# Optimization experiments

Measured on AMD Instinct MI355X. Metric: run time of the kernel, lower is better.

The kernel has to match this reference:

```python
import jax, jax.numpy as jnp
import numpy as np

B, Hh, Ww, C = 16, 56, 56, 256
NH, WS, SS = 8, 7, 3
HD = C // NH
N = WS * WS
SCALE = HD ** -0.5
EPS = 1e-5


def _rel_pos_index():
    coords = np.stack(np.meshgrid(np.arange(WS), np.arange(WS), indexing='ij'))  # (2, ws, ws)
    cf = coords.reshape(2, -1)
    rc = (cf[:, :, None] - cf[:, None, :]).transpose(1, 2, 0).astype(np.int64)  # (N, N, 2)
    rc[:, :, 0] += WS - 1
    rc[:, :, 1] += WS - 1
    rc[:, :, 0] *= 2 * WS - 1
    return jnp.asarray(rc.sum(-1))  # (N, N)

REL_IDX = _rel_pos_index()


def _shift_mask():
    # standard Swin SW-MSA mask for cyclic shift
    img = np.zeros((1, Hh, Ww, 1), dtype=np.float32)
    cnt = 0
    for hs in (slice(0, -WS), slice(-WS, -SS), slice(-SS, None)):
        for ws_ in (slice(0, -WS), slice(-WS, -SS), slice(-SS, None)):
            img[:, hs, ws_, :] = cnt
            cnt += 1
    mw = img.reshape(1, Hh // WS, WS, Ww // WS, WS, 1).transpose(0, 1, 3, 2, 4, 5).reshape(-1, N)
    am = mw[:, None, :] - mw[:, :, None]
    return jnp.asarray(np.where(am != 0, -100.0, 0.0).astype(np.float32))  # (nW, N, N)


def _ln(x, g, b):
    mu = x.mean(-1, keepdims=True)
    var = ((x - mu) ** 2).mean(-1, keepdims=True)
    return (x - mu) * jax.lax.rsqrt(var + EPS) * g + b


def setup_inputs() -> dict:
    key = jax.random.key(0)
    ks = jax.random.split(key, 8)
    return {
        'x': jax.random.normal(ks[0], (B, Hh * Ww, C), jnp.float32),
        'mask': _shift_mask(),
        'norm1_g': jnp.ones((C,), jnp.float32),
        'norm1_b': jnp.zeros((C,), jnp.float32),
        'qkv_w': jax.random.normal(ks[1], (3 * C, C), jnp.float32) * 0.02,
        'qkv_b': jnp.zeros((3 * C,), jnp.float32),
        'rel_bias': jax.random.normal(ks[2], ((2 * WS - 1) ** 2, NH), jnp.float32) * 0.02,
        'proj_w': jax.random.normal(ks[3], (C, C), jnp.float32) * 0.02,
        'proj_b': jnp.zeros((C,), jnp.float32),
        'norm2_g': jnp.ones((C,), jnp.float32),
        'norm2_b': jnp.zeros((C,), jnp.float32),
        'fc1_w': jax.random.normal(ks[4], (4 * C, C), jnp.float32) * 0.02,
        'fc1_b': jnp.zeros((4 * C,), jnp.float32),
        'fc2_w': jax.random.normal(ks[5], (C, 4 * C), jnp.float32) * 0.02,
        'fc2_b': jnp.zeros((C,), jnp.float32),
    }


def reference(x, mask, norm1_g, norm1_b, qkv_w, qkv_b, rel_bias, proj_w, proj_b,
              norm2_g, norm2_b, fc1_w, fc1_b, fc2_w, fc2_b):
    shortcut = x
    h = _ln(x, norm1_g, norm1_b).reshape(B, Hh, Ww, C)
    # cyclic shift
    h = jnp.roll(h, (-SS, -SS), axis=(1, 2))
    # window partition -> (B*nW, N, C)
    hw = h.reshape(B, Hh // WS, WS, Ww // WS, WS, C).transpose(0, 1, 3, 2, 4, 5).reshape(-1, N, C)
    # qkv projection
    qkv = (hw @ qkv_w.T + qkv_b).reshape(-1, N, 3, NH, HD).transpose(2, 0, 3, 1, 4)
    q, k, v = qkv[0] * SCALE, qkv[1], qkv[2]  # (Bw, NH, N, HD)
    attn = jnp.einsum('bhnd,bhmd->bhnm', q, k)  # (Bw, NH, N, N)
    rpb = rel_bias[REL_IDX.reshape(-1)].reshape(N, N, NH).transpose(2, 0, 1)
    attn = attn + rpb[None]
    nW = mask.shape[0]
    attn = attn.reshape(B, nW, NH, N, N) + mask[None, :, None]
    attn = jax.nn.softmax(attn.reshape(-1, NH, N, N), axis=-1)
    o = jnp.einsum('bhnm,bhmd->bhnd', attn, v).transpose(0, 2, 1, 3).reshape(-1, N, C)
    o = o @ proj_w.T + proj_b
    # window reverse
    o = o.reshape(B, Hh // WS, Ww // WS, WS, WS, C).transpose(0, 1, 3, 2, 4, 5).reshape(B, Hh, Ww, C)
    o = jnp.roll(o, (SS, SS), axis=(1, 2)).reshape(B, Hh * Ww, C)
    x = shortcut + o
    h2 = _ln(x, norm2_g, norm2_b)
    h2 = jax.nn.gelu(h2 @ fc1_w.T + fc1_b, approximate=False)
    return x + (h2 @ fc2_w.T + fc2_b)
```

## Files before the change

kernel.cpp:

```cpp
#include <hip/hip_runtime.h>
#include <cmath>

#define B_    16
#define HH    56
#define WWI   56
#define C_    256
#define NH_   8
#define WS_   7
#define SS_   3
#define HD_   32
#define NTOK  50176
#define NN    49
#define SCALE_ 0.17677669529663689f
#define EPS_  1e-5f

typedef __bf16  bf16x8  __attribute__((ext_vector_type(8)));
typedef float   f32x4   __attribute__((ext_vector_type(4)));
typedef unsigned short ushort8v __attribute__((ext_vector_type(8)));

__device__ __forceinline__ unsigned short f2bf(float f) {
    unsigned int u = __float_as_uint(f);
    unsigned int r = u + 0x7FFFu + ((u >> 16) & 1u);
    return (unsigned short)(r >> 16);
}
__device__ __forceinline__ float bf2f(unsigned short h) {
    return __uint_as_float(((unsigned int)h) << 16);
}
__device__ __forceinline__ float gelu_t(float x) {
    float t = 0.7978845608028654f * (x + 0.044715f * x * x * x);
    float e = __expf(2.0f * t);
    float th = 1.0f - 2.0f * __builtin_amdgcn_rcpf(e + 1.0f);
    return 0.5f * x * (1.0f + th);
}

__device__ __forceinline__ void gload_lds16(const unsigned short* g, unsigned short* l) {
    __builtin_amdgcn_global_load_lds(
        (const __attribute__((address_space(1))) unsigned int*)g,
        (__attribute__((address_space(3))) unsigned int*)l, 16, 0, 0);
}

__global__ __launch_bounds__(256) void prep_k(
    const float* __restrict__ qkvw, const float* __restrict__ projw,
    const float* __restrict__ fc1w, const float* __restrict__ fc2w,
    unsigned short* __restrict__ dst,
    const float* __restrict__ mask, const float* __restrict__ relb,
    unsigned short* __restrict__ cb)
{
    if (blockIdx.x < 3072) {
        int i = blockIdx.x * 256 + threadIdx.x;
        float v;
        if      (i < 196608) v = qkvw[i];
        else if (i < 262144) v = projw[i - 196608];
        else if (i < 524288) v = fc1w[i - 262144];
        else                 v = fc2w[i - 524288];
        dst[i] = f2bf(v);
    } else {
        int s = blockIdx.x - 3072;
        int wi = s >> 3, head = s & 7;
        for (int p = threadIdx.x; p < 2408; p += 256) {
            float v = 0.0f;
            if (p < 2401) {
                int i = p / NN, j = p - i * NN;
                int di = i / 7 - j / 7 + 6, dj = i % 7 - j % 7 + 6;
                v = relb[(di * 13 + dj) * NH_ + head] + mask[(size_t)wi * 2401 + p];
            }
            cb[(size_t)s * 2408 + p] = f2bf(v);
        }
    }
}

__global__ __launch_bounds__(256) void ln_k(
    const float* __restrict__ x, const float* __restrict__ g,
    const float* __restrict__ bta, unsigned short* __restrict__ dst, int shifted)
{
    int wave = threadIdx.x >> 6, lane = threadIdx.x & 63;
    int tok = blockIdx.x * 4 + wave;
    const float4 v = *(const float4*)(x + (size_t)tok * C_ + lane * 4);
    float s = v.x + v.y + v.z + v.w;
    float q = v.x*v.x + v.y*v.y + v.z*v.z + v.w*v.w;
    for (int o = 32; o > 0; o >>= 1) { s += __shfl_xor(s, o, 64); q += __shfl_xor(q, o, 64); }
    float mu  = s * (1.0f / C_);
    float var = q * (1.0f / C_) - mu * mu;
    float rs  = rsqrtf(var + EPS_);
    float4 gg = *(const float4*)(g   + lane * 4);
    float4 bb = *(const float4*)(bta + lane * 4);
    float y0 = (v.x - mu) * rs * gg.x + bb.x;
    float y1 = (v.y - mu) * rs * gg.y + bb.y;
    float y2 = (v.z - mu) * rs * gg.z + bb.z;
    float y3 = (v.w - mu) * rs * gg.w + bb.w;
    size_t di;
    if (shifted) {
        int b = tok / 3136, p = tok % 3136;
        int ph = p / 56, pw = p % 56;
        int sh = ph - SS_; if (sh < 0) sh += HH;
        int sw = pw - SS_; if (sw < 0) sw += WWI;
        int bw = b * 64 + (sh / WS_) * 8 + (sw / WS_);
        int n  = (sh % WS_) * WS_ + (sw % WS_);
        di = ((size_t)bw * NN + n) * C_ + lane * 4;
    } else {
        di = (size_t)tok * C_ + lane * 4;
    }
    unsigned int lo = (unsigned int)f2bf(y0) | ((unsigned int)f2bf(y1) << 16);
    unsigned int hi = (unsigned int)f2bf(y2) | ((unsigned int)f2bf(y3) << 16);
    uint2 u; u.x = lo; u.y = hi;
    *(uint2*)(dst + di) = u;
}

template<int EPI, int NT>
__global__ __launch_bounds__(256, 4) void gemm_k(
    const unsigned short* __restrict__ A, const unsigned short* __restrict__ Bt,
    int K, const float* __restrict__ bias,
    const float* __restrict__ resid, float* __restrict__ outF,
    unsigned short* __restrict__ outQ, unsigned short* __restrict__ outK,
    unsigned short* __restrict__ outV)
{
    __shared__ __align__(16) unsigned char smem[32768];
    const int tid = threadIdx.x;
    const int lin = blockIdx.x;
    const int xcd = lin & 7, t = lin >> 3;
    const int m0 = (xcd * 49 + t / NT) * 128;
    const int n0 = (t % NT) * 128;
    const int wave = tid >> 6, lane = tid & 63, quad = lane >> 4, l16 = lane & 15;
    const int wm = wave >> 1, wn = wave & 1;
    const int r0 = tid >> 2;
    const int c0 = (((tid & 3) ^ ((tid >> 3) & 3)) * 8);

    const size_t gA0 = (size_t)(m0 + r0) * K + c0;
    const size_t gA1 = (size_t)(m0 + r0 + 64) * K + c0;
    const size_t gB0 = (size_t)(n0 + r0) * K + c0;
    const size_t gB1 = (size_t)(n0 + r0 + 64) * K + c0;
    const int woff = wave * 512;
    const int sw8 = (quad ^ ((l16 >> 1) & 3)) * 8;

    f32x4 acc[4][4] = {};
    const int nk = K >> 5;

    #define STAGE(kt_, p_) { \
        unsigned short* sA_ = (unsigned short*)(smem + (p_) * 16384); \
        unsigned short* sB_ = sA_ + 4096; \
        const int kp_ = (kt_) << 5; \
        gload_lds16(A + gA0 + kp_, sA_ + woff); \
        gload_lds16(A + gA1 + kp_, sA_ + woff + 2048); \
        gload_lds16(Bt + gB0 + kp_, sB_ + woff); \
        gload_lds16(Bt + gB1 + kp_, sB_ + woff + 2048); }

    STAGE(0, 0);
    for (int kk = 0; kk < nk; ++kk) {
        const int p = kk & 1;
        if (kk + 1 < nk) {
            STAGE(kk + 1, p ^ 1);
            __asm volatile("s_waitcnt vmcnt(4)\n\ts_barrier" ::: "memory");
        } else {
            __asm volatile("s_waitcnt vmcnt(0)\n\ts_barrier" ::: "memory");
        }
        const unsigned short* sA = (const unsigned short*)(smem + p * 16384);
        const unsigned short* sB = sA + 4096;
        bf16x8 af[4], bfr[4];
        #pragma unroll
        for (int tt = 0; tt < 4; ++tt) {
            af[tt]  = __builtin_bit_cast(bf16x8, *(const ushort8v*)(sA + (wm * 64 + tt * 16 + l16) * 32 + sw8));
            bfr[tt] = __builtin_bit_cast(bf16x8, *(const ushort8v*)(sB + (wn * 64 + tt * 16 + l16) * 32 + sw8));
        }
        #pragma unroll
        for (int mt = 0; mt < 4; ++mt)
            #pragma unroll
            for (int nt = 0; nt < 4; ++nt)
                acc[mt][nt] = __builtin_amdgcn_mfma_f32_16x16x32_bf16(af[mt], bfr[nt], acc[mt][nt], 0, 0, 0);
        __asm volatile("s_barrier" ::: "memory");
    }
    #undef STAGE

    float b4[4];
    #pragma unroll
    for (int nt = 0; nt < 4; ++nt) b4[nt] = bias[n0 + wn * 64 + nt * 16 + l16];

    if (EPI == 0 || EPI == 2) {
        unsigned short (*swB)[136] = (unsigned short (*)[136])smem;
        const int seg = n0 >> 8;
        const float qs = (EPI == 0 && seg == 0) ? SCALE_ : 1.0f;
        #pragma unroll
        for (int p = 0; p < 2; ++p) {
            __syncthreads();
            if (wm == p) {
                #pragma unroll
                for (int mt = 0; mt < 4; ++mt)
                    #pragma unroll
                    for (int nt = 0; nt < 4; ++nt)
                        #pragma unroll
                        for (int r = 0; r < 4; ++r) {
                            float v = acc[mt][nt][r] + b4[nt];
                            if (EPI == 0) v *= qs; else v = gelu_t(v);
                            swB[mt * 16 + quad * 4 + r][wn * 64 + nt * 16 + l16] = f2bf(v);
                        }
            }
            __syncthreads();
            if (EPI == 0) {
                unsigned short* dstp = seg == 0 ? outQ : (seg == 1 ? outK : outV);
                const int nbase = n0 & 255;
                for (int tt = tid; tt < 1024; tt += 256) {
                    int row = tt >> 4, c8 = (tt & 15) * 8;
                    int m = m0 + p * 64 + row, bw = m / NN, nw = m - bw * NN;
                    int cc = nbase + c8;
                    uint4 u = *(uint4*)&swB[row][c8];
                    *(uint4*)&dstp[(((size_t)bw * NH_ + (cc >> 5)) * NN + nw) * HD_ + (cc & 31)] = u;
                }
            } else {
                for (int tt = tid; tt < 1024; tt += 256) {
                    int row = tt >> 4, c8 = (tt & 15) * 8;
                    uint4 u = *(uint4*)&swB[row][c8];
                    *(uint4*)&outQ[(size_t)(m0 + p * 64 + row) * 1024 + n0 + c8] = u;
                }
            }
        }
    } else {
        float (*swF)[132] = (float (*)[132])smem;
        #pragma unroll
        for (int p = 0; p < 4; ++p) {
            __syncthreads();
            if (wm == (p >> 1)) {
                const int mtb = (p & 1) * 2;
                #pragma unroll
                for (int mt = 0; mt < 2; ++mt)
                    #pragma unroll
                    for (int nt = 0; nt < 4; ++nt)
                        #pragma unroll
                        for (int r = 0; r < 4; ++r)
                            swF[mt * 16 + quad * 4 + r][wn * 64 + nt * 16 + l16] =
                                acc[mtb + mt][nt][r] + b4[nt];
            }
            __syncthreads();
            for (int tt = tid; tt < 1024; tt += 256) {
                int rl = tt >> 5, c4 = (tt & 31) * 4;
                size_t adr;
                if (EPI == 1) {
                    int m = m0 + p * 32 + rl, bw = m / NN, nw = m - bw * NN;
                    int b = bw >> 6, wi = bw & 63;
                    int sh = (wi >> 3) * WS_ + nw / WS_;
                    int sw = (wi & 7) * WS_ + nw % WS_;
                    int ph = sh + SS_; if (ph >= HH)  ph -= HH;
                    int pw = sw + SS_; if (pw >= WWI) pw -= WWI;
                    adr = ((size_t)b * 3136 + ph * 56 + pw) * C_ + n0 + c4;
                } else {
                    adr = (size_t)(m0 + p * 32 + rl) * C_ + n0 + c4;
                }
                float4 u = *(float4*)&swF[rl][c4];
                const float4 rr = (EPI == 1) ? *(const float4*)&resid[adr]
                                             : *(const float4*)&outF[adr];
                u.x += rr.x; u.y += rr.y; u.z += rr.z; u.w += rr.w;
                *(float4*)&outF[adr] = u;
            }
        }
    }
}

__global__ __launch_bounds__(256) void attn_k(
    const unsigned short* __restrict__ qb, const unsigned short* __restrict__ kb,
    const unsigned short* __restrict__ vb, const unsigned short* __restrict__ cb,
    unsigned short* __restrict__ ob)
{
    __shared__ unsigned short qs[64][40];
    __shared__ unsigned short ks[64][40];
    __shared__ unsigned short vt[32][72];
    __shared__ unsigned short sp[64][72];
    __shared__ unsigned short cbs[2408];
    const int tid = threadIdx.x;
    const int bw = blockIdx.x >> 3, head = blockIdx.x & 7;
    const size_t base = (size_t)blockIdx.x * (NN * HD_);

    for (int t = tid; t < 588; t += 256) {
        int seg = t / 196, idx = t - seg * 196;
        int e = idx * 8;
        const unsigned short* src = (seg == 0 ? qb : seg == 1 ? kb : vb) + base + e;
        uint4 u = *(const uint4*)src;
        if (seg == 0)      *(uint4*)&qs[e >> 5][e & 31] = u;
        else if (seg == 1) *(uint4*)&ks[e >> 5][e & 31] = u;
        else {
            int n = e >> 5, hd = e & 31;
            const unsigned short* pu = (const unsigned short*)&u;
            #pragma unroll
            for (int uu = 0; uu < 8; ++uu) vt[hd + uu][n] = pu[uu];
        }
    }
    {
        const unsigned short* cbase = cb + (size_t)(((bw & 63) * 8 + head)) * 2408;
        for (int t = tid; t < 301; t += 256)
            *(uint4*)&cbs[t * 8] = *(const uint4*)(cbase + t * 8);
        for (int t = tid; t < 480; t += 256) vt[t / 15][NN + t % 15] = 0;
    }
    __syncthreads();

    const int wave = tid >> 6, lane = tid & 63, quad = lane >> 4, l16 = lane & 15;
    const f32x4 zz = {};

    bf16x8 afq = __builtin_bit_cast(bf16x8, *(const ushort8v*)&qs[wave * 16 + l16][quad * 8]);
    f32x4 s4[4];
    #pragma unroll
    for (int jt = 0; jt < 4; ++jt) {
        bf16x8 bk = __builtin_bit_cast(bf16x8, *(const ushort8v*)&ks[jt * 16 + l16][quad * 8]);
        s4[jt] = __builtin_amdgcn_mfma_f32_16x16x32_bf16(afq, bk, zz, 0, 0, 0);
    }

    #pragma unroll
    for (int r = 0; r < 4; ++r) {
        int i = wave * 16 + quad * 4 + r;
        float vals[4];
        #pragma unroll
        for (int jt = 0; jt < 4; ++jt) {
            int j = jt * 16 + l16;
            vals[jt] = (i < NN && j < NN) ? s4[jt][r] + bf2f(cbs[i * NN + j]) : -1e30f;
        }
        float mx = fmaxf(fmaxf(vals[0], vals[1]), fmaxf(vals[2], vals[3]));
        #pragma unroll
        for (int o = 1; o < 16; o <<= 1) mx = fmaxf(mx, __shfl_xor(mx, o, 64));
        float e[4], sum = 0.0f;
        #pragma unroll
        for (int jt = 0; jt < 4; ++jt) { e[jt] = __expf(vals[jt] - mx); sum += e[jt]; }
        #pragma unroll
        for (int o = 1; o < 16; o <<= 1) sum += __shfl_xor(sum, o, 64);
        float inv = 1.0f / sum;
        #pragma unroll
        for (int jt = 0; jt < 4; ++jt) sp[i][jt * 16 + l16] = f2bf(e[jt] * inv);
    }
    __syncthreads();

    bf16x8 ap[2];
    #pragma unroll
    for (int kt = 0; kt < 2; ++kt)
        ap[kt] = __builtin_bit_cast(bf16x8, *(const ushort8v*)&sp[wave * 16 + l16][kt * 32 + quad * 8]);
    f32x4 o4[2] = {};
    #pragma unroll
    for (int nt = 0; nt < 2; ++nt)
        #pragma unroll
        for (int kt = 0; kt < 2; ++kt) {
            bf16x8 bv = __builtin_bit_cast(bf16x8, *(const ushort8v*)&vt[nt * 16 + l16][kt * 32 + quad * 8]);
            o4[nt] = __builtin_amdgcn_mfma_f32_16x16x32_bf16(ap[kt], bv, o4[nt], 0, 0, 0);
        }
    #pragma unroll
    for (int nt = 0; nt < 2; ++nt)
        #pragma unroll
        for (int r = 0; r < 4; ++r) {
            int i = wave * 16 + quad * 4 + r;
            if (i < NN)
                ob[((size_t)bw * NN + i) * C_ + head * HD_ + nt * 16 + l16] = f2bf(o4[nt][r]);
        }
}

extern "C" void kernel_launch(void* const* d_in, const int* in_sizes, int n_in,
                              void* d_out, int out_size, void* d_ws, size_t ws_size,
                              hipStream_t stream)
{
    const float* x     = (const float*)d_in[0];
    const float* mask  = (const float*)d_in[1];
    const float* n1g   = (const float*)d_in[2];
    const float* n1b   = (const float*)d_in[3];
    const float* qkvw  = (const float*)d_in[4];
    const float* qkvb  = (const float*)d_in[5];
    const float* relb  = (const float*)d_in[6];
    const float* projw = (const float*)d_in[7];
    const float* projb = (const float*)d_in[8];
    const float* n2g   = (const float*)d_in[9];
    const float* n2b   = (const float*)d_in[10];
    const float* fc1w  = (const float*)d_in[11];
    const float* fc1b  = (const float*)d_in[12];
    const float* fc2w  = (const float*)d_in[13];
    const float* fc2b  = (const float*)d_in[14];
    float* out = (float*)d_out;

    unsigned short* wq = (unsigned short*)d_ws;
    unsigned short* wp = wq + 196608;
    unsigned short* w1 = wq + 262144;
    unsigned short* w2 = wq + 524288;
    unsigned short* hw = wq + 786432;
    unsigned short* qb = hw + 12845056;
    unsigned short* kb = qb + 12845056;
    unsigned short* vb = kb + 12845056;
    unsigned short* ob = vb + 12845056;
    unsigned short* h2 = ob + 12845056;
    unsigned short* a1 = h2 + 12845056;
    unsigned short* cbt = a1;

    prep_k<<<3584, 256, 0, stream>>>(qkvw, projw, fc1w, fc2w, wq, mask, relb, cbt);
    ln_k<<<12544, 256, 0, stream>>>(x, n1g, n1b, hw, 1);
    gemm_k<0, 6><<<392 * 6, 256, 0, stream>>>(hw, wq, 256, qkvb, nullptr, nullptr, qb, kb, vb);
    attn_k<<<8192, 256, 0, stream>>>(qb, kb, vb, cbt, ob);
    gemm_k<1, 2><<<392 * 2, 256, 0, stream>>>(ob, wp, 256, projb, x, out, nullptr, nullptr, nullptr);
    ln_k<<<12544, 256, 0, stream>>>(out, n2g, n2b, h2, 0);
    gemm_k<2, 8><<<392 * 8, 256, 0, stream>>>(h2, w1, 256, fc1b, nullptr, nullptr, a1, nullptr, nullptr);
    gemm_k<3, 2><<<392 * 2, 256, 0, stream>>>(a1, w2, 1024, fc2b, nullptr, out, nullptr, nullptr, nullptr);
}
```

Measured before the change: 372.9 us.

## Fuse proj GEMM with residual and LayerNorm2; add triple-buffered fc1 GEMM

A new projln_k kernel computes the attention projection with a full 256-column tile per block. It adds the residual in the window-reverse order, writes the fp32 output, then applies LayerNorm2 per row and writes the bf16 h2, so the separate ln_k pass over the output is no longer needed. fc1 moves to a dedicated gemm3_k with a three-stage LDS pipeline and a single-pass GELU epilogue. The fc2 epilogue now stages results through bf16 LDS instead of fp32 before the residual add, which saves LDS traffic but rounds the MLP output to bf16. Using larger tiles and 48KB of LDS in the fused kernels may reduce occupancy, and projln_k launches only 392 blocks.

```diff
diff --git a/kernel.cpp b/kernel.cpp
--- a/kernel.cpp
+++ b/kernel.cpp
@@ -71,7 +71,7 @@
 
 __global__ __launch_bounds__(256) void ln_k(
     const float* __restrict__ x, const float* __restrict__ g,
-    const float* __restrict__ bta, unsigned short* __restrict__ dst, int shifted)
+    const float* __restrict__ bta, unsigned short* __restrict__ dst)
 {
     int wave = threadIdx.x >> 6, lane = threadIdx.x & 63;
     int tok = blockIdx.x * 4 + wave;
@@ -88,18 +88,13 @@
     float y1 = (v.y - mu) * rs * gg.y + bb.y;
     float y2 = (v.z - mu) * rs * gg.z + bb.z;
     float y3 = (v.w - mu) * rs * gg.w + bb.w;
-    size_t di;
-    if (shifted) {
-        int b = tok / 3136, p = tok % 3136;
-        int ph = p / 56, pw = p % 56;
-        int sh = ph - SS_; if (sh < 0) sh += HH;
-        int sw = pw - SS_; if (sw < 0) sw += WWI;
-        int bw = b * 64 + (sh / WS_) * 8 + (sw / WS_);
-        int n  = (sh % WS_) * WS_ + (sw % WS_);
-        di = ((size_t)bw * NN + n) * C_ + lane * 4;
-    } else {
-        di = (size_t)tok * C_ + lane * 4;
-    }
+    int b = tok / 3136, p = tok % 3136;
+    int ph = p / 56, pw = p % 56;
+    int sh = ph - SS_; if (sh < 0) sh += HH;
+    int sw = pw - SS_; if (sw < 0) sw += WWI;
+    int bw = b * 64 + (sh / WS_) * 8 + (sw / WS_);
+    int n  = (sh % WS_) * WS_ + (sw % WS_);
+    size_t di = ((size_t)bw * NN + n) * C_ + lane * 4;
     unsigned int lo = (unsigned int)f2bf(y0) | ((unsigned int)f2bf(y1) << 16);
     unsigned int hi = (unsigned int)f2bf(y2) | ((unsigned int)f2bf(y3) << 16);
     uint2 u; u.x = lo; u.y = hi;
@@ -174,81 +169,263 @@
     #pragma unroll
     for (int nt = 0; nt < 4; ++nt) b4[nt] = bias[n0 + wn * 64 + nt * 16 + l16];
 
-    if (EPI == 0 || EPI == 2) {
-        unsigned short (*swB)[136] = (unsigned short (*)[136])smem;
-        const int seg = n0 >> 8;
-        const float qs = (EPI == 0 && seg == 0) ? SCALE_ : 1.0f;
-        #pragma unroll
-        for (int p = 0; p < 2; ++p) {
-            __syncthreads();
-            if (wm == p) {
+    unsigned short (*swB)[136] = (unsigned short (*)[136])smem;
+    const int seg = n0 >> 8;
+    const float qs = (EPI == 0 && seg == 0) ? SCALE_ : 1.0f;
+    #pragma unroll
+    for (int p = 0; p < 2; ++p) {
+        __syncthreads();
+        if (wm == p) {
+            #pragma unroll
+            for (int mt = 0; mt < 4; ++mt)
                 #pragma unroll
-                for (int mt = 0; mt < 4; ++mt)
+                for (int nt = 0; nt < 4; ++nt)
                     #pragma unroll
-                    for (int nt = 0; nt < 4; ++nt)
-                        #pragma unroll
-                        for (int r = 0; r < 4; ++r) {
-                            float v = acc[mt][nt][r] + b4[nt];
-                            if (EPI == 0) v *= qs; else v = gelu_t(v);
-                            swB[mt * 16 + quad * 4 + r][wn * 64 + nt * 16 + l16] = f2bf(v);
-                        }
+                    for (int r = 0; r < 4; ++r) {
+                        float v = acc[mt][nt][r] + b4[nt];
+                        if (EPI == 0) v *= qs;
+                        swB[mt * 16 + quad * 4 + r][wn * 64 + nt * 16 + l16] = f2bf(v);
+                    }
+        }
+        __syncthreads();
+        if (EPI == 0) {
+            unsigned short* dstp = seg == 0 ? outQ : (seg == 1 ? outK : outV);
+            const int nbase = n0 & 255;
+            for (int tt = tid; tt < 1024; tt += 256) {
+                int row = tt >> 4, c8 = (tt & 15) * 8;
+                int m = m0 + p * 64 + row, bw = m / NN, nw = m - bw * NN;
+                int cc = nbase + c8;
+                uint4 u = *(uint4*)&swB[row][c8];
+                *(uint4*)&dstp[(((size_t)bw * NH_ + (cc >> 5)) * NN + nw) * HD_ + (cc & 31)] = u;
             }
-            __syncthreads();
-            if (EPI == 0) {
-                unsigned short* dstp = seg == 0 ? outQ : (seg == 1 ? outK : outV);
-                const int nbase = n0 & 255;
-                for (int tt = tid; tt < 1024; tt += 256) {
-                    int row = tt >> 4, c8 = (tt & 15) * 8;
-                    int m = m0 + p * 64 + row, bw = m / NN, nw = m - bw * NN;
-                    int cc = nbase + c8;
-                    uint4 u = *(uint4*)&swB[row][c8];
-                    *(uint4*)&dstp[(((size_t)bw * NH_ + (cc >> 5)) * NN + nw) * HD_ + (cc & 31)] = u;
-                }
-            } else {
-                for (int tt = tid; tt < 1024; tt += 256) {
-                    int row = tt >> 4, c8 = (tt & 15) * 8;
-                    uint4 u = *(uint4*)&swB[row][c8];
-                    *(uint4*)&outQ[(size_t)(m0 + p * 64 + row) * 1024 + n0 + c8] = u;
-                }
+        } else {
+            for (int tt = tid; tt < 1024; tt += 256) {
+                int row = tt >> 4, c8 = (tt & 15) * 8;
+                size_t adr = (size_t)(m0 + p * 64 + row) * C_ + n0 + c8;
+                float4 u0, u1;
+                unsigned short* sp8 = &swB[row][c8];
+                u0.x = bf2f(sp8[0]); u0.y = bf2f(sp8[1]); u0.z = bf2f(sp8[2]); u0.w = bf2f(sp8[3]);
+                u1.x = bf2f(sp8[4]); u1.y = bf2f(sp8[5]); u1.z = bf2f(sp8[6]); u1.w = bf2f(sp8[7]);
+                const float4 r0_ = *(const float4*)&outF[adr];
+                const float4 r1_ = *(const float4*)&outF[adr + 4];
+                u0.x += r0_.x; u0.y += r0_.y; u0.z += r0_.z; u0.w += r0_.w;
+                u1.x += r1_.x; u1.y += r1_.y; u1.z += r1_.z; u1.w += r1_.w;
+                *(float4*)&outF[adr] = u0;
+                *(float4*)&outF[adr + 4] = u1;
             }
         }
-    } else {
-        float (*swF)[132] = (float (*)[132])smem;
-        #pragma unroll
-        for (int p = 0; p < 4; ++p) {
-            __syncthreads();
-            if (wm == (p >> 1)) {
-                const int mtb = (p & 1) * 2;
+    }
+}
+
+template<int NT>
+__global__ __launch_bounds__(256) void gemm3_k(
+    const unsigned short* __restrict__ A, const unsigned short* __restrict__ Bt,
+    int K, const float* __restrict__ bias, unsigned short* __restrict__ outB)
+{
+    __shared__ __align__(16) unsigned char smem[49152];
+    const int tid = threadIdx.x;
+    const int lin = blockIdx.x;
+    const int xcd = lin & 7, t = lin >> 3;
+    const int m0 = (xcd * 49 + t / NT) * 128;
+    const int n0 = (t % NT) * 128;
+    const int wave = tid >> 6, lane = tid & 63, quad = lane >> 4, l16 = lane & 15;
+    const int wm = wave >> 1, wn = wave & 1;
+    const int r0 = tid >> 2;
+    const int c0 = (((tid & 3) ^ ((tid >> 3) & 3)) * 8);
+
+    const size_t gA0 = (size_t)(m0 + r0) * K + c0;
+    const size_t gA1 = (size_t)(m0 + r0 + 64) * K + c0;
+    const size_t gB0 = (size_t)(n0 + r0) * K + c0;
+    const size_t gB1 = (size_t)(n0 + r0 + 64) * K + c0;
+    const int woff = wave * 512;
+    const int sw8 = (quad ^ ((l16 >> 1) & 3)) * 8;
+
+    f32x4 acc[4][4] = {};
+    const int nk = K >> 5;
+    #pragma unroll
+    for (int p = 0; p < 2; ++p) {
+        unsigned short* sA = (unsigned short*)(smem + p * 16384);
+        unsigned short* sB = sA + 4096;
+        const int kp = p << 5;
+        gload_lds16(A + gA0 + kp, sA + woff);
+        gload_lds16(A + gA1 + kp, sA + woff + 2048);
+        gload_lds16(Bt + gB0 + kp, sB + woff);
+        gload_lds16(Bt + gB1 + kp, sB + woff + 2048);
+    }
+    int bufc = 0;
+    for (int kk = 0; kk < nk; ++kk) {
+        if (kk + 2 < nk) {
+            int bufn = bufc + 2; if (bufn >= 3) bufn -= 3;
+            unsigned short* sA = (unsigned short*)(smem + bufn * 16384);
+            unsigned short* sB = sA + 4096;
+            const int k2 = (kk + 2) << 5;
+            gload_lds16(A + gA0 + k2, sA + woff);
+            gload_lds16(A + gA1 + k2, sA + woff + 2048);
+            gload_lds16(Bt + gB0 + k2, sB + woff);
+            gload_lds16(Bt + gB1 + k2, sB + woff + 2048);
+            __asm volatile("s_waitcnt vmcnt(8)\n\ts_barrier" ::: "memory");
+        } else if (kk + 1 < nk) {
+            __asm volatile("s_waitcnt vmcnt(4)\n\ts_barrier" ::: "memory");
+        } else {
+            __asm volatile("s_waitcnt vmcnt(0)\n\ts_barrier" ::: "memory");
+        }
+        const unsigned short* sA = (const unsigned short*)(smem + bufc * 16384);
+        const unsigned short* sB = sA + 4096;
+        bf16x8 af[4], bfr[4];
+        #pragma unroll
+        for (int tt = 0; tt < 4; ++tt) {
+            af[tt]  = __builtin_bit_cast(bf16x8, *(const ushort8v*)(sA + (wm * 64 + tt * 16 + l16) * 32 + sw8));
+            bfr[tt] = __builtin_bit_cast(bf16x8, *(const ushort8v*)(sB + (wn * 64 + tt * 16 + l16) * 32 + sw8));
+        }
+        #pragma unroll
+        for (int mt = 0; mt < 4; ++mt)
+            #pragma unroll
+            for (int nt = 0; nt < 4; ++nt)
+                acc[mt][nt] = __builtin_amdgcn_mfma_f32_16x16x32_bf16(af[mt], bfr[nt], acc[mt][nt], 0, 0, 0);
+        __asm volatile("s_barrier" ::: "memory");
+        if (++bufc == 3) bufc = 0;
+    }
+
+    float b4[4];
+    #pragma unroll
+    for (int nt = 0; nt < 4; ++nt) b4[nt] = bias[n0 + wn * 64 + nt * 16 + l16];
+
+    unsigned short (*swB)[136] = (unsigned short (*)[136])smem;
+    #pragma unroll
+    for (int mt = 0; mt < 4; ++mt)
+        #pragma unroll
+        for (int nt = 0; nt < 4; ++nt)
+            #pragma unroll
+            for (int r = 0; r < 4; ++r) {
+                float v = gelu_t(acc[mt][nt][r] + b4[nt]);
+                swB[wm * 64 + mt * 16 + quad * 4 + r][wn * 64 + nt * 16 + l16] = f2bf(v);
+            }
+    __syncthreads();
+    for (int tt = tid; tt < 2048; tt += 256) {
+        int row = tt >> 4, c8 = (tt & 15) * 8;
+        uint4 u = *(uint4*)&swB[row][c8];
+        *(uint4*)&outB[(size_t)(m0 + row) * 1024 + n0 + c8] = u;
+    }
+}
+
+__global__ __launch_bounds__(256) void projln_k(
+    const unsigned short* __restrict__ A, const unsigned short* __restrict__ Bt,
+    const float* __restrict__ bias, const float* __restrict__ resid,
+    const float* __restrict__ g2, const float* __restrict__ b2,
+    float* __restrict__ outF, unsigned short* __restrict__ h2)
+{
+    __shared__ __align__(16) unsigned char smem[49152];
+    const int tid = threadIdx.x;
+    const int lin = blockIdx.x;
+    const int xcd = lin & 7, t = lin >> 3;
+    const int m0 = (xcd * 49 + t) * 128;
+    const int wave = tid >> 6, lane = tid & 63, quad = lane >> 4, l16 = lane & 15;
+    const int wm = wave >> 1, wn = wave & 1;
+    const int r0 = tid >> 2;
+    const int c0 = (((tid & 3) ^ ((tid >> 3) & 3)) * 8);
+    const int K = 256;
+    const size_t gA0 = (size_t)(m0 + r0) * K + c0;
+    const size_t gA1 = (size_t)(m0 + r0 + 64) * K + c0;
+    const size_t gB0 = (size_t)(r0)       * K + c0;
+    const size_t gB1 = (size_t)(r0 + 64)  * K + c0;
+    const size_t gB2 = (size_t)(r0 + 128) * K + c0;
+    const size_t gB3 = (size_t)(r0 + 192) * K + c0;
+    const int woff = wave * 512;
+    const int sw8 = (quad ^ ((l16 >> 1) & 3)) * 8;
+
+    f32x4 acc[4][8] = {};
+    const int nk = 8;
+
+    #define PSTG(kt_, p_) { \
+        unsigned short* sA_ = (unsigned short*)(smem + (p_) * 24576); \
+        unsigned short* sB_ = sA_ + 4096; \
+        const int kp_ = (kt_) << 5; \
+        gload_lds16(A  + gA0 + kp_, sA_ + woff); \
+        gload_lds16(A  + gA1 + kp_, sA_ + woff + 2048); \
+        gload_lds16(Bt + gB0 + kp_, sB_ + woff); \
+        gload_lds16(Bt + gB1 + kp_, sB_ + woff + 2048); \
+        gload_lds16(Bt + gB2 + kp_, sB_ + woff + 4096); \
+        gload_lds16(Bt + gB3 + kp_, sB_ + woff + 6144); }
+
+    PSTG(0, 0);
+    for (int kk = 0; kk < nk; ++kk) {
+        const int p = kk & 1;
+        if (kk + 1 < nk) {
+            PSTG(kk + 1, p ^ 1);
+            __asm volatile("s_waitcnt vmcnt(6)\n\ts_barrier" ::: "memory");
+        } else {
+            __asm volatile("s_waitcnt vmcnt(0)\n\ts_barrier" ::: "memory");
+        }
+        const unsigned short* sA = (const unsigned short*)(smem + p * 24576);
+        const unsigned short* sB = sA + 4096;
+        bf16x8 af[4], bfr[8];
+        #pragma unroll
+        for (int tt = 0; tt < 4; ++tt)
+            af[tt]  = __builtin_bit_cast(bf16x8, *(const ushort8v*)(sA + (wm * 64 + tt * 16 + l16) * 32 + sw8));
+        #pragma unroll
+        for (int nt = 0; nt < 8; ++nt)
+            bfr[nt] = __builtin_bit_cast(bf16x8, *(const ushort8v*)(sB + (wn * 128 + nt * 16 + l16) * 32 + sw8));
+        #pragma unroll
+        for (int mt = 0; mt < 4; ++mt)
+            #pragma unroll
+            for (int nt = 0; nt < 8; ++nt)
+                acc[mt][nt] = __builtin_amdgcn_mfma_f32_16x16x32_bf16(af[mt], bfr[nt], acc[mt][nt], 0, 0, 0);
+        __asm volatile("s_barrier" ::: "memory");
+    }
+    #undef PSTG
+
+    float b8[8];
+    #pragma unroll
+    for (int nt = 0; nt < 8; ++nt) b8[nt] = bias[wn * 128 + nt * 16 + l16];
+    const float4 g4  = *(const float4*)&g2[lane * 4];
+    const float4 bb4 = *(const float4*)&b2[lane * 4];
+
+    float (*swF)[260] = (float (*)[260])smem;
+    #pragma unroll
+    for (int p = 0; p < 4; ++p) {
+        __syncthreads();
+        if (wm == (p >> 1)) {
+            const int mtb = (p & 1) * 2;
+            #pragma unroll
+            for (int mt = 0; mt < 2; ++mt)
                 #pragma unroll
-                for (int mt = 0; mt < 2; ++mt)
+                for (int nt = 0; nt < 8; ++nt)
                     #pragma unroll
-                    for (int nt = 0; nt < 4; ++nt)
-                        #pragma unroll
-                        for (int r = 0; r < 4; ++r)
-                            swF[mt * 16 + quad * 4 + r][wn * 64 + nt * 16 + l16] =
-                                acc[mtb + mt][nt][r] + b4[nt];
-            }
-            __syncthreads();
-            for (int tt = tid; tt < 1024; tt += 256) {
-                int rl = tt >> 5, c4 = (tt & 31) * 4;
-                size_t adr;
-                if (EPI == 1) {
-                    int m = m0 + p * 32 + rl, bw = m / NN, nw = m - bw * NN;
-                    int b = bw >> 6, wi = bw & 63;
-                    int sh = (wi >> 3) * WS_ + nw / WS_;
-                    int sw = (wi & 7) * WS_ + nw % WS_;
-                    int ph = sh + SS_; if (ph >= HH)  ph -= HH;
-                    int pw = sw + SS_; if (pw >= WWI) pw -= WWI;
-                    adr = ((size_t)b * 3136 + ph * 56 + pw) * C_ + n0 + c4;
-                } else {
-                    adr = (size_t)(m0 + p * 32 + rl) * C_ + n0 + c4;
-                }
-                float4 u = *(float4*)&swF[rl][c4];
-                const float4 rr = (EPI == 1) ? *(const float4*)&resid[adr]
-                                             : *(const float4*)&outF[adr];
-                u.x += rr.x; u.y += rr.y; u.z += rr.z; u.w += rr.w;
-                *(float4*)&outF[adr] = u;
-            }
+                    for (int r = 0; r < 4; ++r)
+                        swF[mt * 16 + quad * 4 + r][wn * 128 + nt * 16 + l16] =
+                            acc[mtb + mt][nt][r] + b8[nt];
+        }
+        __syncthreads();
+        #pragma unroll
+        for (int i = 0; i < 8; ++i) {
+            int r32 = i * 4 + wave;
+            int m = m0 + p * 32 + r32;
+            int bw = m / NN, nw = m - bw * NN;
+            int b = bw >> 6, wi = bw & 63;
+            int sh = (wi >> 3) * WS_ + nw / WS_;
+            int sw = (wi & 7) * WS_ + nw % WS_;
+            int ph = sh + SS_; if (ph >= HH)  ph -= HH;
+            int pw = sw + SS_; if (pw >= WWI) pw -= WWI;
+            size_t rowadr = ((size_t)b * 3136 + ph * 56 + pw) * C_;
+            float4 v = *(float4*)&swF[r32][lane * 4];
+            const float4 rr = *(const float4*)&resid[rowadr + lane * 4];
+            v.x += rr.x; v.y += rr.y; v.z += rr.z; v.w += rr.w;
+            *(float4*)&outF[rowadr + lane * 4] = v;
+            float s = v.x + v.y + v.z + v.w;
+            float q = v.x*v.x + v.y*v.y + v.z*v.z + v.w*v.w;
+            #pragma unroll
+            for (int o = 32; o > 0; o >>= 1) { s += __shfl_xor(s, o, 64); q += __shfl_xor(q, o, 64); }
+            float mu  = s * (1.0f / C_);
+            float var = q * (1.0f / C_) - mu * mu;
+            float rs  = rsqrtf(var + EPS_);
+            float y0 = (v.x - mu) * rs * g4.x + bb4.x;
+            float y1 = (v.y - mu) * rs * g4.y + bb4.y;
+            float y2 = (v.z - mu) * rs * g4.z + bb4.z;
+            float y3 = (v.w - mu) * rs * g4.w + bb4.w;
+            unsigned int lo = (unsigned int)f2bf(y0) | ((unsigned int)f2bf(y1) << 16);
+            unsigned int hi = (unsigned int)f2bf(y2) | ((unsigned int)f2bf(y3) << 16);
+            uint2 uu; uu.x = lo; uu.y = hi;
+            *(uint2*)&h2[rowadr + lane * 4] = uu;
         }
     }
 }
@@ -380,11 +557,10 @@
     unsigned short* cbt = a1;
 
     prep_k<<<3584, 256, 0, stream>>>(qkvw, projw, fc1w, fc2w, wq, mask, relb, cbt);
-    ln_k<<<12544, 256, 0, stream>>>(x, n1g, n1b, hw, 1);
+    ln_k<<<12544, 256, 0, stream>>>(x, n1g, n1b, hw);
     gemm_k<0, 6><<<392 * 6, 256, 0, stream>>>(hw, wq, 256, qkvb, nullptr, nullptr, qb, kb, vb);
     attn_k<<<8192, 256, 0, stream>>>(qb, kb, vb, cbt, ob);
-    gemm_k<1, 2><<<392 * 2, 256, 0, stream>>>(ob, wp, 256, projb, x, out, nullptr, nullptr, nullptr);
-    ln_k<<<12544, 256, 0, stream>>>(out, n2g, n2b, h2, 0);
-    gemm_k<2, 8><<<392 * 8, 256, 0, stream>>>(h2, w1, 256, fc1b, nullptr, nullptr, a1, nullptr, nullptr);
+    projln_k<<<392, 256, 0, stream>>>(ob, wp, projb, x, n2g, n2b, out, h2);
+    gemm3_k<8><<<392 * 8, 256, 0, stream>>>(h2, w1, 256, fc1b, a1);
     gemm_k<3, 2><<<392 * 2, 256, 0, stream>>>(a1, w2, 1024, fc2b, nullptr, out, nullptr, nullptr, nullptr);
 }
```

Result: slower. 387.8 us (+4.0%).
